# Kernel optimization log

Measured on AMD Instinct MI355X. Metric: run time of the kernel, lower is better.

Reference implementation:

```python
import jax, jax.numpy as jnp
import numpy as np

Z, K, H, Y = 128, 256, 512, 4  # z_size, key_size, hidden_size, y_dim


def setup_inputs() -> dict:
    key = jax.random.key(0)
    ks = jax.random.split(key, 8)
    B, T, P = 512, 32, 32
    s = lambda k, shape, sc: (jax.random.normal(k, shape, jnp.float32) * sc)
    return {
        "x_seq": jax.random.normal(ks[0], (B, T, P, P), jnp.float32),
        "W_enc": s(ks[1], (P * P, Z), 0.03),
        "gamma": jnp.ones((Z,), jnp.float32),
        "beta": jnp.zeros((Z,), jnp.float32),
        "W_ih": s(ks[2], (4 * H, K + 1), 0.05),
        "W_hh": s(ks[3], (4 * H, H), 0.04),
        "b_ih": jnp.zeros((4 * H,), jnp.float32),
        "b_hh": jnp.zeros((4 * H,), jnp.float32),
        "W_key": s(ks[4], (K, H), 0.06),
        "b_key": jnp.zeros((K,), jnp.float32),
        "W_g": s(ks[5], (1, H), 0.06),
        "b_g": jnp.zeros((1,), jnp.float32),
        "conf_gain": jnp.ones((1,), jnp.float32),
        "conf_bias": jnp.zeros((1,), jnp.float32),
        "W_y": s(ks[6], (Y, H), 0.06),
        "b_y": jnp.zeros((Y,), jnp.float32),
    }


def _lstm_cell(x, h, c, W_ih, W_hh, b_ih, b_hh):
    # PyTorch gate order: i, f, g, o
    gates = x @ W_ih.T + b_ih + h @ W_hh.T + b_hh
    i, f, g, o = jnp.split(gates, 4, axis=-1)
    c = jax.nn.sigmoid(f) * c + jax.nn.sigmoid(i) * jnp.tanh(g)
    h = jax.nn.sigmoid(o) * jnp.tanh(c)
    return h, c


def _forward(x_seq, W_enc, gamma, beta, W_ih, W_hh, b_ih, b_hh,
             W_key, b_key, W_g, b_g, conf_gain, conf_bias, W_y, b_y):
    B, T, P, _ = x_seq.shape
    # encoder: flatten -> linear to z_size (stand-in for Encoder_mlp)
    z = x_seq.reshape(B, T, P * P) @ W_enc  # [B, T, Z]
    # context norm over the sequence dim (single task segment)
    mu = z.mean(axis=1, keepdims=True)
    sig = jnp.sqrt(z.var(axis=1, keepdims=True) + 1e-8)
    z = (z - mu) / sig * gamma + beta

    M = T + 1  # T+1 steps; final step feeds a zero z_t
    z_pad = jnp.concatenate([z, jnp.zeros((B, 1, Z), z.dtype)], axis=1)  # [B, M, Z]

    h0 = jnp.zeros((B, H), z.dtype)
    c0 = jnp.zeros((B, H), z.dtype)
    kr0 = jnp.zeros((B, K + 1), z.dtype)
    Mk0 = jnp.zeros((B, M, K), z.dtype)
    Mv0 = jnp.zeros((B, M, Z), z.dtype)

    def step(carry, t):
        h, c, key_r, M_k, M_v = carry
        z_t = jax.lax.dynamic_index_in_dim(z_pad, t, axis=1, keepdims=False)  # [B, Z]
        h, c = _lstm_cell(key_r, h, c, W_ih, W_hh, b_ih, b_hh)
        key_w = jax.nn.relu(h @ W_key.T + b_key)          # [B, K]
        g = jax.nn.sigmoid(h @ W_g.T + b_g)               # [B, 1]
        y_lin = h @ W_y.T + b_y                            # [B, Y]
        # attention read over valid memory slots j < t
        scores = jnp.einsum('bz,bmz->bm', z_t, M_v)        # [B, M]
        valid = (jnp.arange(M) < t)[None, :]
        w_k = jax.nn.softmax(jnp.where(valid, scores, -1e9), axis=1)
        c_k = jax.nn.sigmoid(scores * conf_gain + conf_bias)
        kv = jnp.concatenate([M_k, c_k[..., None]], axis=2)  # [B, M, K+1]
        attn = g * jnp.einsum('bm,bmd->bd', w_k, kv)          # [B, K+1]
        key_r_new = jnp.where(t == 0, jnp.zeros_like(attn), attn)
        # append to memory at slot t
        M_k = jax.lax.dynamic_update_slice_in_dim(M_k, key_w[:, None, :], t, axis=1)
        M_v = jax.lax.dynamic_update_slice_in_dim(M_v, z_t[:, None, :], t, axis=1)
        return (h, c, key_r_new, M_k, M_v), y_lin

    _, ys = jax.lax.scan(step, (h0, c0, kr0, Mk0, Mv0), jnp.arange(M))
    return ys[-1]  # y_pred_linear from final step, [B, Y]


def reference(x_seq, W_enc, gamma, beta, W_ih, W_hh, b_ih, b_hh,
              W_key, b_key, W_g, b_g, conf_gain, conf_bias, W_y, b_y):
    y_pred_linear = _forward(x_seq, W_enc, gamma, beta, W_ih, W_hh, b_ih, b_hh,
                             W_key, b_key, W_g, b_g, conf_gain, conf_bias, W_y, b_y)
    y_pred = jnp.argmax(y_pred_linear, axis=1)
    return y_pred_linear, y_pred
```

## Files before the change

### kernel.cpp

```cpp
#include <hip/hip_runtime.h>
#include <math.h>

typedef unsigned short ushort;
typedef unsigned int uint;
typedef __bf16 bf16x8 __attribute__((ext_vector_type(8)));
typedef float f32x4 __attribute__((ext_vector_type(4)));

#define ZS    128
#define KS    256
#define HS    512
#define BATCH 512
#define TT    32
#define MM    33
#define NB    2304
#define KPAD  800
#define HOFF  272
#define LDA   800

static __device__ __forceinline__ float sigf(float x) { return 1.f / (1.f + expf(-x)); }
static __device__ __forceinline__ float bf2f(ushort u) { return __uint_as_float((uint)u << 16); }

__global__ void prep_w(const float* __restrict__ W_ih, const float* __restrict__ W_hh,
                       const float* __restrict__ W_key, const float* __restrict__ b_ih,
                       const float* __restrict__ b_hh, const float* __restrict__ b_key,
                       const float* __restrict__ W_enc,
                       ushort* __restrict__ Whi, ushort* __restrict__ Wlo,
                       ushort* __restrict__ Behi, ushort* __restrict__ Belo,
                       float* __restrict__ biasN)
{
    int idx = blockIdx.x * 256 + threadIdx.x;
    if (idx < NB) {
        float bv;
        if (idx < 2048) { int j = idx >> 2, gi = idx & 3, r = gi * 512 + j; bv = b_ih[r] + b_hh[r]; }
        else bv = b_key[idx - 2048];
        biasN[idx] = bv;
    }
    if (idx < NB * KPAD) {
        int n = idx / KPAD, k = idx - n * KPAD;
        float v = 0.f;
        if (n < 2048) {
            int j = n >> 2, gi = n & 3, r = gi * 512 + j;
            if (k < 257) v = W_ih[r * 257 + k];
            else if (k >= HOFF && k < HOFF + 512) v = W_hh[r * 512 + (k - HOFF)];
        } else {
            if (k >= HOFF && k < HOFF + 512) v = W_key[(n - 2048) * 512 + (k - HOFF)];
        }
        uint u = __float_as_uint(v);
        Whi[idx] = (ushort)(u >> 16);
        float lo = v - __uint_as_float(u & 0xFFFF0000u);
        Wlo[idx] = (ushort)(__float_as_uint(lo) >> 16);
    } else if (idx < NB * KPAD + 128 * 1024) {
        int e = idx - NB * KPAD;
        int n = e >> 10, k = e & 1023;
        float v = W_enc[k * 128 + n];
        uint u = __float_as_uint(v);
        Behi[e] = (ushort)(u >> 16);
        float lo = v - __uint_as_float(u & 0xFFFF0000u);
        Belo[e] = (ushort)(__float_as_uint(lo) >> 16);
    }
}

template<int BN, int MODE, bool PRESPLIT>
__global__ __launch_bounds__(256, (MODE == 1) ? 5 : 4)
void gemm_mfma(const float* __restrict__ A,
               const ushort* __restrict__ Ahi, const ushort* __restrict__ Alo, int lda,
               const ushort* __restrict__ Bhi, const ushort* __restrict__ Blo, int ldb,
               int nslice,
               float* __restrict__ out,
               float* __restrict__ out2)
{
    constexpr int NI = BN / 32;
    constexpr int AHI = 0, ALO = 32 * 40, BHI = 64 * 40, BLO = 64 * 40 + BN * 40;
    constexpr int BUF = 64 * 40 + 2 * BN * 40;
    __shared__ ushort lds[2 * BUF];

    const int tid = threadIdx.x;
    int bx, by, kb, kc;
    if (MODE == 1) {
        int wg = blockIdx.x;
        int swz = (wg & 7) * 144 + (wg >> 3);
        int zz = swz / 576;
        int r  = swz - zz * 576;
        bx = r >> 4; by = r & 15;
        kb = zz ? 13 : 0;
        kc = zz ? 12 : 13;
        if (zz) out = out2;
    } else {
        bx = blockIdx.x; by = blockIdx.y;
        kb = 0; kc = nslice;
    }
    const int row0 = by * 32, n0 = bx * BN;
    const int l = tid & 63, w = tid >> 6, wm = w >> 1, wn = w & 1;
    const int lm = l & 15, kg = (l >> 4) << 3;

    f32x4 acc[NI];
    const f32x4 zero4 = {0.f, 0.f, 0.f, 0.f};
#pragma unroll
    for (int ni = 0; ni < NI; ni++) acc[ni] = zero4;

    float4 avf;
    uint4 avu;
    uint4 bhv[BN / 64], blv[BN / 64];

    auto LOADG = [&](int a) {
        const int k0 = a * 32;
        if (PRESPLIT) {
            int idx = tid & 127, r = idx >> 2, c = (idx & 3) << 3;
            const ushort* src = (tid < 128) ? Ahi : Alo;
            avu = *(const uint4*)(src + (size_t)(row0 + r) * lda + k0 + c);
        } else {
            int r = tid >> 3, c = (tid & 7) << 2;
            avf = *(const float4*)(A + (size_t)(row0 + r) * lda + k0 + c);
        }
#pragma unroll
        for (int i = 0; i < BN / 64; i++) {
            int idx = tid + 256 * i, r = idx >> 2, c = (idx & 3) << 3;
            bhv[i] = *(const uint4*)(Bhi + (size_t)(n0 + r) * ldb + k0 + c);
            blv[i] = *(const uint4*)(Blo + (size_t)(n0 + r) * ldb + k0 + c);
        }
    };
    auto STORE = [&](int buf) {
        ushort* L = lds + buf * BUF;
        if (PRESPLIT) {
            int idx = tid & 127, r = idx >> 2, c = (idx & 3) << 3;
            *(uint4*)&L[(tid < 128 ? AHI : ALO) + r * 40 + c] = avu;
        } else {
            int r = tid >> 3, c = (tid & 7) << 2;
            uint u0 = __float_as_uint(avf.x), u1 = __float_as_uint(avf.y);
            uint u2 = __float_as_uint(avf.z), u3 = __float_as_uint(avf.w);
            uint hp0 = (u1 & 0xFFFF0000u) | (u0 >> 16);
            uint hp1 = (u3 & 0xFFFF0000u) | (u2 >> 16);
            float l0 = avf.x - __uint_as_float(u0 & 0xFFFF0000u);
            float l1 = avf.y - __uint_as_float(u1 & 0xFFFF0000u);
            float l2 = avf.z - __uint_as_float(u2 & 0xFFFF0000u);
            float l3 = avf.w - __uint_as_float(u3 & 0xFFFF0000u);
            uint lp0 = (__float_as_uint(l1) & 0xFFFF0000u) | (__float_as_uint(l0) >> 16);
            uint lp1 = (__float_as_uint(l3) & 0xFFFF0000u) | (__float_as_uint(l2) >> 16);
            *(uint2*)&L[AHI + r * 40 + c] = make_uint2(hp0, hp1);
            *(uint2*)&L[ALO + r * 40 + c] = make_uint2(lp0, lp1);
        }
#pragma unroll
        for (int i = 0; i < BN / 64; i++) {
            int idx = tid + 256 * i, r = idx >> 2, c = (idx & 3) << 3;
            *(uint4*)&L[BHI + r * 40 + c] = bhv[i];
            *(uint4*)&L[BLO + r * 40 + c] = blv[i];
        }
    };
    auto COMPUTE = [&](int buf) {
        const ushort* L = lds + buf * BUF;
        bf16x8 ah, alv, bh[NI], bl[NI];
        {
            int r = wm * 16 + lm;
            ah  = *(const bf16x8*)&L[AHI + r * 40 + kg];
            alv = *(const bf16x8*)&L[ALO + r * 40 + kg];
        }
#pragma unroll
        for (int ni = 0; ni < NI; ni++) {
            int r = wn * (BN / 2) + ni * 16 + lm;
            bh[ni] = *(const bf16x8*)&L[BHI + r * 40 + kg];
            bl[ni] = *(const bf16x8*)&L[BLO + r * 40 + kg];
        }
#pragma unroll
        for (int ni = 0; ni < NI; ni++) {
            acc[ni] = __builtin_amdgcn_mfma_f32_16x16x32_bf16(ah,  bh[ni], acc[ni], 0, 0, 0);
            acc[ni] = __builtin_amdgcn_mfma_f32_16x16x32_bf16(ah,  bl[ni], acc[ni], 0, 0, 0);
            acc[ni] = __builtin_amdgcn_mfma_f32_16x16x32_bf16(alv, bh[ni], acc[ni], 0, 0, 0);
        }
    };

    LOADG(kb);
    STORE(0);
    for (int s = 0; s < kc; s++) {
        if (s + 1 < kc) LOADG(kb + s + 1);
        __syncthreads();
        COMPUTE(s & 1);
        if (s + 1 < kc) STORE((s + 1) & 1);
    }

    const int crow = (l >> 4) << 2;
    if (MODE == 0) {
#pragma unroll
        for (int ni = 0; ni < NI; ni++)
#pragma unroll
            for (int r = 0; r < 4; r++) {
                int m = row0 + wm * 16 + crow + r;
                int z = n0 + wn * (BN / 2) + ni * 16 + lm;
                out[(size_t)(m >> 5) * (MM * ZS) + (m & 31) * ZS + z] = acc[ni][r];
            }
    } else {
#pragma unroll
        for (int ni = 0; ni < NI; ni++)
#pragma unroll
            for (int r = 0; r < 4; r++) {
                int b = row0 + wm * 16 + crow + r;
                int n = n0 + wn * (BN / 2) + ni * 16 + lm;
                out[(size_t)b * NB + n] = acc[ni][r];
            }
    }
}

__global__ __launch_bounds__(256)
void cell_k(const float* __restrict__ P0, const float* __restrict__ P1,
            const float* __restrict__ biasN, float* __restrict__ cst,
            ushort* __restrict__ outHi, ushort* __restrict__ outLo,
            float* __restrict__ Mk,
            const float* __restrict__ W_g, const float* __restrict__ b_g,
            const float* __restrict__ watt, const float* __restrict__ wc,
            int t)
{
    __shared__ float hsh[512];
    __shared__ float red[256];
    __shared__ float wts[32];
    __shared__ float gsh;
    int b = blockIdx.x, tid = threadIdx.x;
    const float* p0 = P0 + (size_t)b * NB;
    const float* p1 = P1 + (size_t)b * NB;
    ushort* rHi = outHi + (size_t)b * LDA;
    ushort* rLo = outLo + (size_t)b * LDA;
#pragma unroll
    for (int u = 0; u < 2; u++) {
        int j = tid + u * 256;
        float4 a  = *(const float4*)(p0 + 4 * j);
        float4 c4 = *(const float4*)(p1 + 4 * j);
        float4 bb = *(const float4*)(biasN + 4 * j);
        float gi = a.x + c4.x + bb.x;
        float gf = a.y + c4.y + bb.y;
        float gg = a.z + c4.z + bb.z;
        float go = a.w + c4.w + bb.w;
        float iv = sigf(gi), fv = sigf(gf), gv = tanhf(gg), ov = sigf(go);
        float cn = fv * cst[(size_t)b * HS + j] + iv * gv;
        float hv = ov * tanhf(cn);
        cst[(size_t)b * HS + j] = cn;
        hsh[j] = hv;
        uint uu = __float_as_uint(hv);
        rHi[HOFF + j] = (ushort)(uu >> 16);
        float lo = hv - __uint_as_float(uu & 0xFFFF0000u);
        rLo[HOFF + j] = (ushort)(__float_as_uint(lo) >> 16);
    }
    float kv = fmaxf(p0[2048 + tid] + p1[2048 + tid] + biasN[2048 + tid], 0.f);
    if (t >= 1) Mk[((size_t)(t - 1) * BATCH + b) * KS + tid] = kv;
    if (t < 1 || t > 31) return;
    if (tid < t) wts[tid] = watt[(b * MM + t) * MM + tid];
    __syncthreads();
    red[tid] = hsh[tid] * W_g[tid] + hsh[tid + 256] * W_g[tid + 256];
    __syncthreads();
    for (int s = 128; s > 0; s >>= 1) {
        if (tid < s) red[tid] += red[tid + s];
        __syncthreads();
    }
    if (tid == 0) gsh = sigf(red[0] + b_g[0]);
    __syncthreads();
    float g = gsh;
    float acc = wts[t - 1] * kv;
    for (int m = 0; m < t - 1; m++)
        acc += wts[m] * Mk[((size_t)m * BATCH + b) * KS + tid];
    float v = g * acc;
    uint u2 = __float_as_uint(v);
    rHi[tid] = (ushort)(u2 >> 16);
    float lo2 = v - __uint_as_float(u2 & 0xFFFF0000u);
    rLo[tid] = (ushort)(__float_as_uint(lo2) >> 16);
    if (tid == 0) {
        float vc = g * wc[b * MM + t];
        uint uc = __float_as_uint(vc);
        rHi[256] = (ushort)(uc >> 16);
        float lc = vc - __uint_as_float(uc & 0xFFFF0000u);
        rLo[256] = (ushort)(__float_as_uint(lc) >> 16);
    }
}

__global__ void norm_k(float* __restrict__ z_pad, const float* __restrict__ gamma,
                       const float* __restrict__ beta)
{
    int b = blockIdx.x, zc = threadIdx.x;
    float* zb = z_pad + (size_t)b * (MM * ZS);
    float s = 0.f, s2 = 0.f;
    for (int t = 0; t < TT; t++) { float v = zb[t * ZS + zc]; s += v; s2 += v * v; }
    float mu = s * (1.f / 32.f);
    float var = s2 * (1.f / 32.f) - mu * mu;
    float rstd = 1.f / sqrtf(var + 1e-8f);
    float ga = gamma[zc], be = beta[zc];
    for (int t = 0; t < TT; t++) {
        float v = zb[t * ZS + zc];
        zb[t * ZS + zc] = (v - mu) * rstd * ga + be;
    }
    zb[TT * ZS + zc] = 0.f;
}

__global__ __launch_bounds__(256)
void scores_k(const float* __restrict__ z_pad, const float* __restrict__ cg_p,
              const float* __restrict__ cb_p, float* __restrict__ watt,
              float* __restrict__ wc)
{
    __shared__ float zs[MM * 129];
    int b = blockIdx.x, tid = threadIdx.x;
    const float* zb = z_pad + (size_t)b * (MM * ZS);
    for (int i = tid; i < MM * ZS; i += 256) {
        int m = i >> 7, k = i & 127;
        zs[m * 129 + k] = zb[i];
    }
    __syncthreads();
    float cg = cg_p[0], cb = cb_p[0];
    int wid = tid >> 6, lane = tid & 63;
    for (int t = 1 + wid; t <= 32; t += 4) {
        int m = lane;
        float s = -3.0e38f;
        if (m < t) {
            const float* zt = &zs[t * 129];
            const float* zm = &zs[m * 129];
            float acc = 0.f;
#pragma unroll 8
            for (int k = 0; k < ZS; k++) acc += zt[k] * zm[k];
            s = acc;
        }
        float mx = s;
        for (int off = 1; off < 64; off <<= 1) mx = fmaxf(mx, __shfl_xor(mx, off));
        float e = (m < t) ? expf(s - mx) : 0.f;
        float sum = e;
        for (int off = 1; off < 64; off <<= 1) sum += __shfl_xor(sum, off);
        float w = e / sum;
        if (m < t) watt[(b * MM + t) * MM + m] = w;
        float p = (m < t) ? w * sigf(s * cg + cb) : 0.f;
        for (int off = 1; off < 64; off <<= 1) p += __shfl_xor(p, off);
        if (lane == 0) wc[b * MM + t] = p;
    }
}

__global__ void y_k(const ushort* __restrict__ inpHi, const ushort* __restrict__ inpLo,
                    const float* __restrict__ W_y, const float* __restrict__ b_y,
                    float* __restrict__ out)
{
    int b = blockIdx.x, lane = threadIdx.x;
    const ushort* hHi = inpHi + (size_t)b * LDA + HOFF;
    const ushort* hLo = inpLo + (size_t)b * LDA + HOFF;
    float a0 = 0, a1 = 0, a2 = 0, a3 = 0;
    for (int r = 0; r < 8; r++) {
        int k = lane + r * 64;
        float hv = bf2f(hHi[k]) + bf2f(hLo[k]);
        a0 += hv * W_y[k];
        a1 += hv * W_y[512 + k];
        a2 += hv * W_y[1024 + k];
        a3 += hv * W_y[1536 + k];
    }
    for (int off = 32; off > 0; off >>= 1) {
        a0 += __shfl_xor(a0, off);
        a1 += __shfl_xor(a1, off);
        a2 += __shfl_xor(a2, off);
        a3 += __shfl_xor(a3, off);
    }
    if (lane == 0) {
        float y0 = a0 + b_y[0], y1 = a1 + b_y[1], y2 = a2 + b_y[2], y3 = a3 + b_y[3];
        out[b * 4 + 0] = y0; out[b * 4 + 1] = y1; out[b * 4 + 2] = y2; out[b * 4 + 3] = y3;
        int best = 0; float bv = y0;
        if (y1 > bv) { bv = y1; best = 1; }
        if (y2 > bv) { bv = y2; best = 2; }
        if (y3 > bv) { bv = y3; best = 3; }
        out[2048 + b] = (float)best;
    }
}

extern "C" void kernel_launch(void* const* d_in, const int* in_sizes, int n_in,
                              void* d_out, int out_size, void* d_ws, size_t ws_size,
                              hipStream_t stream)
{
    const float* x_seq = (const float*)d_in[0];
    const float* W_enc = (const float*)d_in[1];
    const float* gamma = (const float*)d_in[2];
    const float* beta  = (const float*)d_in[3];
    const float* W_ih  = (const float*)d_in[4];
    const float* W_hh  = (const float*)d_in[5];
    const float* b_ih  = (const float*)d_in[6];
    const float* b_hh  = (const float*)d_in[7];
    const float* W_key = (const float*)d_in[8];
    const float* b_key = (const float*)d_in[9];
    const float* W_g   = (const float*)d_in[10];
    const float* b_g   = (const float*)d_in[11];
    const float* cgain = (const float*)d_in[12];
    const float* cbias = (const float*)d_in[13];
    const float* W_y   = (const float*)d_in[14];
    const float* b_y   = (const float*)d_in[15];

    float* ws    = (float*)d_ws;
    float* z_pad = ws;
    float* watt  = z_pad + 2162688;
    float* wcv   = watt + 557568;
    float* Mk    = wcv + 16896;
    float* biasN = Mk + 4194304;
    float* cst   = biasN + 2304;
    ushort* inpHi0 = (ushort*)(cst + 262144);
    ushort* inpLo0 = inpHi0 + 409600;
    ushort* inpHi1 = inpLo0 + 409600;
    ushort* inpLo1 = inpHi1 + 409600;
    ushort* Whi  = inpLo1 + 409600;
    ushort* Wlo  = Whi + NB * KPAD;
    ushort* Behi = Wlo + NB * KPAD;
    ushort* Belo = Behi + 131072;
    float* P0 = (float*)(Belo + 131072);
    float* P1 = P0 + (size_t)BATCH * NB;

    hipMemsetAsync(cst, 0, 262144 * sizeof(float) + 4 * 409600 * sizeof(ushort), stream);

    prep_w<<<(NB * KPAD + 131072 + 255) / 256, 256, 0, stream>>>(
        W_ih, W_hh, W_key, b_ih, b_hh, b_key, W_enc, Whi, Wlo, Behi, Belo, biasN);

    gemm_mfma<128, 0, false><<<dim3(1, 512), 256, 0, stream>>>(
        x_seq, nullptr, nullptr, 1024, Behi, Belo, 1024, 32,
        z_pad, nullptr);
    norm_k<<<512, 128, 0, stream>>>(z_pad, gamma, beta);
    scores_k<<<512, 256, 0, stream>>>(z_pad, cgain, cbias, watt, wcv);

    for (int t = 0; t <= 32; t++) {
        ushort* inHiC = (t & 1) ? inpHi1 : inpHi0;
        ushort* inLoC = (t & 1) ? inpLo1 : inpLo0;
        ushort* inHiN = (t & 1) ? inpHi0 : inpHi1;
        ushort* inLoN = (t & 1) ? inpLo0 : inpLo1;
        gemm_mfma<64, 1, true><<<dim3(1152), 256, 0, stream>>>(
            nullptr, inHiC, inLoC, LDA, Whi, Wlo, KPAD, 25,
            P0, P1);
        cell_k<<<512, 256, 0, stream>>>(P0, P1, biasN, cst, inHiN, inLoN,
                                        Mk, W_g, b_g, watt, wcv, t);
    }
    y_k<<<512, 64, 0, stream>>>(inpHi1, inpLo1, W_y, b_y, (float*)d_out);
}
```

Before: 1.011 ms.

## Use 64x64 tiles in the per-step recurrent GEMM with split-K

The per-step gate GEMM moves from 32x64 tiles (1152 workgroups) to 64x64 tiles with a 2x2 MFMA sub-tile per wave (576 workgroups), still split along K into two partial outputs. Each A and B fragment is now reused across two MFMAs, and each workgroup loads less data from global memory per unit of work. The template is split into dedicated encoder and step kernels. The cost is fewer workgroups, which lowers occupancy and parallelism across the GPU, plus a different swizzle mapping.

```diff
diff --git a/kernel.cpp b/kernel.cpp
--- a/kernel.cpp
+++ b/kernel.cpp
@@ -60,36 +60,18 @@
     }
 }
 
-template<int BN, int MODE, bool PRESPLIT>
-__global__ __launch_bounds__(256, (MODE == 1) ? 5 : 4)
-void gemm_mfma(const float* __restrict__ A,
-               const ushort* __restrict__ Ahi, const ushort* __restrict__ Alo, int lda,
-               const ushort* __restrict__ Bhi, const ushort* __restrict__ Blo, int ldb,
-               int nslice,
-               float* __restrict__ out,
-               float* __restrict__ out2)
-{
-    constexpr int NI = BN / 32;
+__global__ __launch_bounds__(256, 4)
+void gemm_enc(const float* __restrict__ A,
+              const ushort* __restrict__ Bhi, const ushort* __restrict__ Blo,
+              float* __restrict__ out)
+{
+    constexpr int BN = 128, NI = 4;
     constexpr int AHI = 0, ALO = 32 * 40, BHI = 64 * 40, BLO = 64 * 40 + BN * 40;
     constexpr int BUF = 64 * 40 + 2 * BN * 40;
     __shared__ ushort lds[2 * BUF];
-
     const int tid = threadIdx.x;
-    int bx, by, kb, kc;
-    if (MODE == 1) {
-        int wg = blockIdx.x;
-        int swz = (wg & 7) * 144 + (wg >> 3);
-        int zz = swz / 576;
-        int r  = swz - zz * 576;
-        bx = r >> 4; by = r & 15;
-        kb = zz ? 13 : 0;
-        kc = zz ? 12 : 13;
-        if (zz) out = out2;
-    } else {
-        bx = blockIdx.x; by = blockIdx.y;
-        kb = 0; kc = nslice;
-    }
-    const int row0 = by * 32, n0 = bx * BN;
+    const int row0 = blockIdx.x * 32, n0 = 0;
+    const int lda = 1024, ldb = 1024, nslice = 32;
     const int l = tid & 63, w = tid >> 6, wm = w >> 1, wn = w & 1;
     const int lm = l & 15, kg = (l >> 4) << 3;
 
@@ -99,51 +81,39 @@
     for (int ni = 0; ni < NI; ni++) acc[ni] = zero4;
 
     float4 avf;
-    uint4 avu;
     uint4 bhv[BN / 64], blv[BN / 64];
 
-    auto LOADG = [&](int a) {
-        const int k0 = a * 32;
-        if (PRESPLIT) {
-            int idx = tid & 127, r = idx >> 2, c = (idx & 3) << 3;
-            const ushort* src = (tid < 128) ? Ahi : Alo;
-            avu = *(const uint4*)(src + (size_t)(row0 + r) * lda + k0 + c);
-        } else {
-            int r = tid >> 3, c = (tid & 7) << 2;
-            avf = *(const float4*)(A + (size_t)(row0 + r) * lda + k0 + c);
-        }
+    auto LOADG = [&](int s) {
+        const int k0 = s * 32;
+        int r = tid >> 3, c = (tid & 7) << 2;
+        avf = *(const float4*)(A + (size_t)(row0 + r) * lda + k0 + c);
 #pragma unroll
         for (int i = 0; i < BN / 64; i++) {
-            int idx = tid + 256 * i, r = idx >> 2, c = (idx & 3) << 3;
-            bhv[i] = *(const uint4*)(Bhi + (size_t)(n0 + r) * ldb + k0 + c);
-            blv[i] = *(const uint4*)(Blo + (size_t)(n0 + r) * ldb + k0 + c);
+            int idx = tid + 256 * i, r2 = idx >> 2, c2 = (idx & 3) << 3;
+            bhv[i] = *(const uint4*)(Bhi + (size_t)(n0 + r2) * ldb + k0 + c2);
+            blv[i] = *(const uint4*)(Blo + (size_t)(n0 + r2) * ldb + k0 + c2);
         }
     };
     auto STORE = [&](int buf) {
         ushort* L = lds + buf * BUF;
-        if (PRESPLIT) {
-            int idx = tid & 127, r = idx >> 2, c = (idx & 3) << 3;
-            *(uint4*)&L[(tid < 128 ? AHI : ALO) + r * 40 + c] = avu;
-        } else {
-            int r = tid >> 3, c = (tid & 7) << 2;
-            uint u0 = __float_as_uint(avf.x), u1 = __float_as_uint(avf.y);
-            uint u2 = __float_as_uint(avf.z), u3 = __float_as_uint(avf.w);
-            uint hp0 = (u1 & 0xFFFF0000u) | (u0 >> 16);
-            uint hp1 = (u3 & 0xFFFF0000u) | (u2 >> 16);
-            float l0 = avf.x - __uint_as_float(u0 & 0xFFFF0000u);
-            float l1 = avf.y - __uint_as_float(u1 & 0xFFFF0000u);
-            float l2 = avf.z - __uint_as_float(u2 & 0xFFFF0000u);
-            float l3 = avf.w - __uint_as_float(u3 & 0xFFFF0000u);
-            uint lp0 = (__float_as_uint(l1) & 0xFFFF0000u) | (__float_as_uint(l0) >> 16);
-            uint lp1 = (__float_as_uint(l3) & 0xFFFF0000u) | (__float_as_uint(l2) >> 16);
-            *(uint2*)&L[AHI + r * 40 + c] = make_uint2(hp0, hp1);
-            *(uint2*)&L[ALO + r * 40 + c] = make_uint2(lp0, lp1);
-        }
+        int r = tid >> 3, c = (tid & 7) << 2;
+        uint u0 = __float_as_uint(avf.x), u1 = __float_as_uint(avf.y);
+        uint u2 = __float_as_uint(avf.z), u3 = __float_as_uint(avf.w);
+        uint hp0 = (u1 & 0xFFFF0000u) | (u0 >> 16);
+        uint hp1 = (u3 & 0xFFFF0000u) | (u2 >> 16);
+        float l0 = avf.x - __uint_as_float(u0 & 0xFFFF0000u);
+        float l1 = avf.y - __uint_as_float(u1 & 0xFFFF0000u);
+        float l2 = avf.z - __uint_as_float(u2 & 0xFFFF0000u);
+        float l3 = avf.w - __uint_as_float(u3 & 0xFFFF0000u);
+        uint lp0 = (__float_as_uint(l1) & 0xFFFF0000u) | (__float_as_uint(l0) >> 16);
+        uint lp1 = (__float_as_uint(l3) & 0xFFFF0000u) | (__float_as_uint(l2) >> 16);
+        *(uint2*)&L[AHI + r * 40 + c] = make_uint2(hp0, hp1);
+        *(uint2*)&L[ALO + r * 40 + c] = make_uint2(lp0, lp1);
 #pragma unroll
         for (int i = 0; i < BN / 64; i++) {
-            int idx = tid + 256 * i, r = idx >> 2, c = (idx & 3) << 3;
-            *(uint4*)&L[BHI + r * 40 + c] = bhv[i];
-            *(uint4*)&L[BLO + r * 40 + c] = blv[i];
+            int idx = tid + 256 * i, r2 = idx >> 2, c2 = (idx & 3) << 3;
+            *(uint4*)&L[BHI + r2 * 40 + c2] = bhv[i];
+            *(uint4*)&L[BLO + r2 * 40 + c2] = blv[i];
         }
     };
     auto COMPUTE = [&](int buf) {
@@ -168,6 +138,93 @@
         }
     };
 
+    LOADG(0);
+    STORE(0);
+    for (int s = 0; s < nslice; s++) {
+        if (s + 1 < nslice) LOADG(s + 1);
+        __syncthreads();
+        COMPUTE(s & 1);
+        if (s + 1 < nslice) STORE((s + 1) & 1);
+    }
+
+    const int crow = (l >> 4) << 2;
+#pragma unroll
+    for (int ni = 0; ni < NI; ni++)
+#pragma unroll
+        for (int r = 0; r < 4; r++) {
+            int m = row0 + wm * 16 + crow + r;
+            int z = n0 + wn * (BN / 2) + ni * 16 + lm;
+            out[(size_t)(m >> 5) * (MM * ZS) + (m & 31) * ZS + z] = acc[ni][r];
+        }
+}
+
+__global__ __launch_bounds__(256, 4)
+void gemm_step(const ushort* __restrict__ Ahi, const ushort* __restrict__ Alo,
+               const ushort* __restrict__ Whi, const ushort* __restrict__ Wlo,
+               float* __restrict__ P0, float* __restrict__ P1)
+{
+    constexpr int AHI = 0, ALO = 64 * 40, BHI = 128 * 40, BLO = 192 * 40;
+    constexpr int BUF = 256 * 40;
+    __shared__ ushort lds[2 * BUF];
+    const int tid = threadIdx.x;
+    int wg = blockIdx.x;
+    int swz = (wg & 7) * 72 + (wg >> 3);
+    int zz = swz / 288;
+    int rr = swz - zz * 288;
+    const int bx = rr >> 3, by = rr & 7;
+    const int kb = zz ? 13 : 0, kc = zz ? 12 : 13;
+    float* __restrict__ out = zz ? P1 : P0;
+    const int row0 = by * 64, n0 = bx * 64;
+    const int l = tid & 63, w = tid >> 6, wm = w >> 1, wn = w & 1;
+    const int lm = l & 15, kg = (l >> 4) << 3;
+    const int ar = tid >> 2, ac = (tid & 3) << 3;
+
+    f32x4 acc[2][2];
+    const f32x4 zero4 = {0.f, 0.f, 0.f, 0.f};
+    acc[0][0] = zero4; acc[0][1] = zero4; acc[1][0] = zero4; acc[1][1] = zero4;
+
+    uint4 av0, av1, bv0, bv1;
+
+    auto LOADG = [&](int a) {
+        const int k0 = a * 32;
+        av0 = *(const uint4*)(Ahi + (size_t)(row0 + ar) * LDA + k0 + ac);
+        av1 = *(const uint4*)(Alo + (size_t)(row0 + ar) * LDA + k0 + ac);
+        bv0 = *(const uint4*)(Whi + (size_t)(n0 + ar) * KPAD + k0 + ac);
+        bv1 = *(const uint4*)(Wlo + (size_t)(n0 + ar) * KPAD + k0 + ac);
+    };
+    auto STORE = [&](int buf) {
+        ushort* L = lds + buf * BUF;
+        int off = ar * 40 + ac;
+        *(uint4*)&L[AHI + off] = av0;
+        *(uint4*)&L[ALO + off] = av1;
+        *(uint4*)&L[BHI + off] = bv0;
+        *(uint4*)&L[BLO + off] = bv1;
+    };
+    auto COMPUTE = [&](int buf) {
+        const ushort* L = lds + buf * BUF;
+        bf16x8 ah[2], al[2], bh[2], bl[2];
+#pragma unroll
+        for (int mi = 0; mi < 2; mi++) {
+            int r = wm * 32 + mi * 16 + lm;
+            ah[mi] = *(const bf16x8*)&L[AHI + r * 40 + kg];
+            al[mi] = *(const bf16x8*)&L[ALO + r * 40 + kg];
+        }
+#pragma unroll
+        for (int ni = 0; ni < 2; ni++) {
+            int r = wn * 32 + ni * 16 + lm;
+            bh[ni] = *(const bf16x8*)&L[BHI + r * 40 + kg];
+            bl[ni] = *(const bf16x8*)&L[BLO + r * 40 + kg];
+        }
+#pragma unroll
+        for (int mi = 0; mi < 2; mi++)
+#pragma unroll
+            for (int ni = 0; ni < 2; ni++) {
+                acc[mi][ni] = __builtin_amdgcn_mfma_f32_16x16x32_bf16(ah[mi], bh[ni], acc[mi][ni], 0, 0, 0);
+                acc[mi][ni] = __builtin_amdgcn_mfma_f32_16x16x32_bf16(ah[mi], bl[ni], acc[mi][ni], 0, 0, 0);
+                acc[mi][ni] = __builtin_amdgcn_mfma_f32_16x16x32_bf16(al[mi], bh[ni], acc[mi][ni], 0, 0, 0);
+            }
+    };
+
     LOADG(kb);
     STORE(0);
     for (int s = 0; s < kc; s++) {
@@ -178,25 +235,16 @@
     }
 
     const int crow = (l >> 4) << 2;
-    if (MODE == 0) {
-#pragma unroll
-        for (int ni = 0; ni < NI; ni++)
+#pragma unroll
+    for (int mi = 0; mi < 2; mi++)
+#pragma unroll
+        for (int ni = 0; ni < 2; ni++)
 #pragma unroll
             for (int r = 0; r < 4; r++) {
-                int m = row0 + wm * 16 + crow + r;
-                int z = n0 + wn * (BN / 2) + ni * 16 + lm;
-                out[(size_t)(m >> 5) * (MM * ZS) + (m & 31) * ZS + z] = acc[ni][r];
+                int b = row0 + wm * 32 + mi * 16 + crow + r;
+                int n = n0 + wn * 32 + ni * 16 + lm;
+                out[(size_t)b * NB + n] = acc[mi][ni][r];
             }
-    } else {
-#pragma unroll
-        for (int ni = 0; ni < NI; ni++)
-#pragma unroll
-            for (int r = 0; r < 4; r++) {
-                int b = row0 + wm * 16 + crow + r;
-                int n = n0 + wn * (BN / 2) + ni * 16 + lm;
-                out[(size_t)b * NB + n] = acc[ni][r];
-            }
-    }
 }
 
 __global__ __launch_bounds__(256)
@@ -402,9 +450,7 @@
     prep_w<<<(NB * KPAD + 131072 + 255) / 256, 256, 0, stream>>>(
         W_ih, W_hh, W_key, b_ih, b_hh, b_key, W_enc, Whi, Wlo, Behi, Belo, biasN);
 
-    gemm_mfma<128, 0, false><<<dim3(1, 512), 256, 0, stream>>>(
-        x_seq, nullptr, nullptr, 1024, Behi, Belo, 1024, 32,
-        z_pad, nullptr);
+    gemm_enc<<<512, 256, 0, stream>>>(x_seq, Behi, Belo, z_pad);
     norm_k<<<512, 128, 0, stream>>>(z_pad, gamma, beta);
     scores_k<<<512, 256, 0, stream>>>(z_pad, cgain, cbias, watt, wcv);
 
@@ -413,9 +459,7 @@
         ushort* inLoC = (t & 1) ? inpLo1 : inpLo0;
         ushort* inHiN = (t & 1) ? inpHi0 : inpHi1;
         ushort* inLoN = (t & 1) ? inpLo0 : inpLo1;
-        gemm_mfma<64, 1, true><<<dim3(1152), 256, 0, stream>>>(
-            nullptr, inHiC, inLoC, LDA, Whi, Wlo, KPAD, 25,
-            P0, P1);
+        gemm_step<<<576, 256, 0, stream>>>(inHiC, inLoC, Whi, Wlo, P0, P1);
         cell_k<<<512, 256, 0, stream>>>(P0, P1, biasN, cst, inHiN, inLoN,
                                         Mk, W_g, b_g, watt, wcv, t);
     }
```

Result: faster. 940.4 us (-7.0%).
